# Kernel tuning notes

Hardware: AMD Instinct MI355X
Metric: run time of the kernel (lower is better)

## Reference

```python
import jax, jax.numpy as jnp
import numpy as np

B, N, D, H = 256, 1000, 128, 8
DH = D // H
TANH_CLIP = 10.0
NEG = -1e9  # finite stand-in for -inf mask fill (keeps grads clean)


def setup_inputs() -> dict:
    key = jax.random.key(0)
    ks = jax.random.split(key, 8)
    s = 1.0 / np.sqrt(D)
    return {
        "node_embeddings": jax.random.normal(ks[0], (B, N, D), jnp.float32),
        "W_node": jax.random.normal(ks[1], (D, 3 * D), jnp.float32) * s,   # project_node_embeddings
        "W_fixed": jax.random.normal(ks[2], (D, D), jnp.float32) * s,      # project_fixed_context
        "W_step": jax.random.normal(ks[3], (2 * D, D), jnp.float32) * s,   # project_step_context
        "W_out": jax.random.normal(ks[4], (D, D), jnp.float32) * s,        # project_out
        "prev_idx": jax.random.randint(ks[5], (B,), 0, N),
        "first_idx": jax.random.randint(ks[6], (B,), 0, N),
        "mask": jax.random.randint(ks[7], (B, N), 0, 2).astype(bool),      # True = masked/visited
    }


def reference(node_embeddings, W_node, W_fixed, W_step, W_out, prev_idx, first_idx, mask):
    b = jnp.arange(B)
    # Precompute fixed: context projection of graph embedding (mean aggregation)
    graph_embed = node_embeddings.mean(axis=1)                    # (B, D)
    fixed_context = graph_embed @ W_fixed                          # (B, D)
    # glimpse key / glimpse val / logit key from node embeddings
    kvl = node_embeddings @ W_node                                 # (B, N, 3D)
    glimpse_K, glimpse_V, logit_K = jnp.split(kvl, 3, axis=-1)
    gK = glimpse_K.reshape(B, N, H, DH)                            # (B, N, H, dh)
    gV = glimpse_V.reshape(B, N, H, DH)
    # Step context: cat(first node embed, last node embed) -> query
    step_ctx = jnp.concatenate(
        [node_embeddings[b, first_idx], node_embeddings[b, prev_idx]], axis=-1)  # (B, 2D)
    query = fixed_context + step_ctx @ W_step                      # (B, D)
    Q = query.reshape(B, H, DH)                                    # (B, H, dh)
    # Glimpse MHA (single query per batch element)
    compat = jnp.einsum("bhd,bnhd->bhn", Q, gK) / np.sqrt(DH)      # (B, H, N)
    compat = jnp.where(mask[:, None, :], NEG, compat)              # mask_inner
    attn = jax.nn.softmax(compat, axis=-1)
    heads = jnp.einsum("bhn,bnhd->bhd", attn, gV)                  # (B, H, dh)
    glimpse = heads.reshape(B, D) @ W_out                          # (B, D)
    # Logits against logit_K, tanh clipping, mask_logits, log-softmax
    logits = jnp.einsum("bd,bnd->bn", glimpse, logit_K) / np.sqrt(D)
    logits = TANH_CLIP * jnp.tanh(logits)
    logits = jnp.where(mask, NEG, logits)
    log_p = jax.nn.log_softmax(logits, axis=-1)                    # (B, N)
    return log_p
```

## Files before the change

### kernel.cpp

```cpp
#include <hip/hip_runtime.h>
#include <math.h>

#define BB 256
#define NN 1000
#define DD 128
#define HH 8
#define CC 8
#define RC 125
#define NEG -1e9f

__device__ __forceinline__ bool get_mask(const void* m, int flag, size_t idx) {
    if (flag == 1) return ((const int*)m)[idx] != 0;
    if (flag == 2) return ((const float*)m)[idx] != 0.0f;
    return ((const unsigned char*)m)[idx] != 0;
}

__global__ __launch_bounds__(256) void k_mean(
        const float* __restrict__ X, float* __restrict__ partial,
        const unsigned int* __restrict__ maskw, int* __restrict__ flag) {
    int bid = blockIdx.x, tid = threadIdx.x;
    int b = bid >> 3, ch = bid & 7;
    if (bid == 0 && tid < 64) {
        unsigned int a0 = maskw[tid], a1 = maskw[tid + 64],
                     a2 = maskw[tid + 128], a3 = maskw[tid + 192];
        int ii = (a0 <= 1u) && (a1 <= 1u) && (a2 <= 1u) && (a3 <= 1u);
        int ff = (a0 == 0u || a0 == 0x3F800000u) && (a1 == 0u || a1 == 0x3F800000u) &&
                 (a2 == 0u || a2 == 0x3F800000u) && (a3 == 0u || a3 == 0x3F800000u);
        int ai = __all(ii), af = __all(ff);
        if (tid == 0) *flag = ai ? 1 : (af ? 2 : 0);
    }
    int c = tid & 31, s = tid >> 5;
    const float4* Xr = (const float4*)(X + (size_t)b * NN * DD);
    float4 acc = make_float4(0.f, 0.f, 0.f, 0.f);
    int n0 = ch * RC;
    for (int nl = s; nl < RC; nl += 8) {
        float4 v = Xr[(n0 + nl) * 32 + c];
        acc.x += v.x; acc.y += v.y; acc.z += v.z; acc.w += v.w;
    }
    __shared__ float4 red[8][32];
    red[s][c] = acc;
    __syncthreads();
    for (int st = 4; st >= 1; st >>= 1) {
        if (s < st) {
            float4 o = red[s + st][c];
            red[s][c].x += o.x; red[s][c].y += o.y;
            red[s][c].z += o.z; red[s][c].w += o.w;
        }
        __syncthreads();
    }
    if (s == 0) {
        float4 r = red[0][c];
        float* outp = partial + ((size_t)b * CC + ch) * DD + 4 * c;
        outp[0] = r.x; outp[1] = r.y; outp[2] = r.z; outp[3] = r.w;
    }
}

__global__ __launch_bounds__(256) void k_qk(
        const float* __restrict__ X, const float* __restrict__ Wfix,
        const float* __restrict__ Wstep, const float* __restrict__ Wnode,
        const float* __restrict__ partial, const int* __restrict__ prev,
        const int* __restrict__ first, const void* __restrict__ mask,
        const int* __restrict__ flag, float* __restrict__ qkg,
        unsigned short* __restrict__ cidx, int* __restrict__ cnt) {
    int b = blockIdx.x, tid = threadIdx.x;
    const size_t xoff = (size_t)b * NN * DD;
    const int f = *flag;
    __shared__ float ge[DD], sc[2 * DD], qv[DD], qp[2][DD];
    __shared__ int wbase[4];
    __shared__ int s_total;

    if (tid < DD) {
        float g = 0.f;
        #pragma unroll
        for (int ch = 0; ch < CC; ++ch) g += partial[((size_t)b * CC + ch) * DD + tid];
        ge[tid] = g * (1.0f / NN);
    }
    {
        int src = (tid < DD) ? first[b] : prev[b];
        sc[tid] = X[xoff + (size_t)src * DD + (tid & 127)];
    }
    if (tid == 0) s_total = 0;
    __syncthreads();
    int p = tid >> 7, d = tid & 127;
    {
        float a = 0.f;
        #pragma unroll 4
        for (int k = p * 64; k < p * 64 + 64; ++k)      a += ge[k] * Wfix[(size_t)k * DD + d];
        #pragma unroll 4
        for (int k = p * 128; k < p * 128 + 128; ++k)   a += sc[k] * Wstep[(size_t)k * DD + d];
        qp[p][d] = a;
    }
    __syncthreads();
    if (tid < DD) qv[tid] = qp[0][tid] + qp[1][tid];
    __syncthreads();
    {
        const float* wrow = Wnode + (size_t)d * 384;
        #pragma unroll
        for (int h = p * 4; h < p * 4 + 4; ++h) {
            const float4* wr = (const float4*)(wrow + h * 16);
            float a = 0.f;
            #pragma unroll
            for (int j4 = 0; j4 < 4; ++j4) {
                float4 w = wr[j4];
                a += w.x * qv[h * 16 + 4 * j4]     + w.y * qv[h * 16 + 4 * j4 + 1]
                   + w.z * qv[h * 16 + 4 * j4 + 2] + w.w * qv[h * 16 + 4 * j4 + 3];
            }
            qkg[((size_t)b * HH + h) * DD + d] = 0.25f * a;
        }
    }
    int w = tid >> 6, lane = tid & 63;
    for (int seg = 0; seg < 4; ++seg) {
        int n = seg * 256 + tid;
        bool un = (n < NN) && !get_mask(mask, f, (size_t)b * NN + n);
        unsigned long long bal = __ballot(un);
        if (lane == 0) wbase[w] = __popcll(bal);
        __syncthreads();
        int base = s_total;
        for (int ww = 0; ww < w; ++ww) base += wbase[ww];
        int myoff = __popcll(bal & ((1ULL << lane) - 1ULL));
        if (un) cidx[(size_t)b * 1024 + base + myoff] = (unsigned short)n;
        __syncthreads();
        if (tid == 0) s_total += wbase[0] + wbase[1] + wbase[2] + wbase[3];
        __syncthreads();
    }
    if (tid == 0) cnt[b] = s_total;
}

__global__ __launch_bounds__(256, 4) void k_flash(
        const float* __restrict__ X, const float* __restrict__ qkg,
        const unsigned short* __restrict__ cidx, const int* __restrict__ cnt,
        float* __restrict__ sqw, float* __restrict__ pvp) {
    int bid = blockIdx.x, tid = threadIdx.x;
    int b = bid >> 3, ch = bid & 7;
    const size_t xoff = (size_t)b * NN * DD;

    __shared__ __align__(16) float qks[HH][DD];
    __shared__ __align__(16) float redpv[4][HH][DD];
    __shared__ float redS[4][HH];

    for (int i = tid; i < HH * DD; i += 256)
        qks[i >> 7][i & 127] = qkg[(size_t)b * HH * DD + i];
    __syncthreads();

    const int g = tid & 15;
    const int r = tid >> 4;
    const int w = tid >> 6;

    int total = cnt[b];
    int rpc = (total + CC - 1) / CC;
    int k0 = ch * rpc;
    int k1 = k0 + rpc; if (k1 > total) k1 = total;
    int len = k1 - k0; if (len < 0) len = 0;
    int iters = (len + 15) >> 4;

    float acc[HH][8];
    #pragma unroll
    for (int h = 0; h < HH; ++h)
        #pragma unroll
        for (int j = 0; j < 8; ++j) acc[h][j] = 0.f;
    float S[HH] = {0.f, 0.f, 0.f, 0.f, 0.f, 0.f, 0.f, 0.f};

    for (int it = 0; it < iters; ++it) {
        int k = k0 + it * 16 + r;
        if (k < k1) {
            int n = cidx[(size_t)b * 1024 + k];
            const float4* xr = (const float4*)(X + xoff + (size_t)n * DD + 8 * g);
            float4 v0 = xr[0], v1 = xr[1];
            float v[8] = {v0.x, v0.y, v0.z, v0.w, v1.x, v1.y, v1.z, v1.w};
            float cp[HH];
            #pragma unroll
            for (int h = 0; h < HH; ++h) {
                const float4* qr = (const float4*)&qks[h][8 * g];
                float4 q0 = qr[0], q1 = qr[1];
                cp[h] = v[0] * q0.x + v[1] * q0.y + v[2] * q0.z + v[3] * q0.w
                      + v[4] * q1.x + v[5] * q1.y + v[6] * q1.z + v[7] * q1.w;
            }
            #pragma unroll
            for (int h = 0; h < HH; ++h) {
                cp[h] += __shfl_xor(cp[h], 1, 16);
                cp[h] += __shfl_xor(cp[h], 2, 16);
                cp[h] += __shfl_xor(cp[h], 4, 16);
                cp[h] += __shfl_xor(cp[h], 8, 16);
            }
            #pragma unroll
            for (int h = 0; h < HH; ++h) {
                float pe = __expf(fminf(cp[h], 80.f));
                S[h] += pe;
                #pragma unroll
                for (int j = 0; j < 8; ++j) acc[h][j] += pe * v[j];
            }
        }
    }
    #pragma unroll
    for (int h = 0; h < HH; ++h) {
        S[h] += __shfl_xor(S[h], 16, 64);
        S[h] += __shfl_xor(S[h], 32, 64);
        #pragma unroll
        for (int j = 0; j < 8; ++j) {
            acc[h][j] += __shfl_xor(acc[h][j], 16, 64);
            acc[h][j] += __shfl_xor(acc[h][j], 32, 64);
        }
    }
    if ((tid & 63) < 16) {
        #pragma unroll
        for (int h = 0; h < HH; ++h) {
            *((float4*)&redpv[w][h][8 * g])     =
                make_float4(acc[h][0], acc[h][1], acc[h][2], acc[h][3]);
            *((float4*)&redpv[w][h][8 * g + 4]) =
                make_float4(acc[h][4], acc[h][5], acc[h][6], acc[h][7]);
        }
        if (g == 0) {
            #pragma unroll
            for (int h = 0; h < HH; ++h) redS[w][h] = S[h];
        }
    }
    __syncthreads();
    for (int idx = tid; idx < HH * DD; idx += 256) {
        int h = idx >> 7, d = idx & 127;
        pvp[(((size_t)b * CC + ch) * HH + h) * DD + d] =
            redpv[0][h][d] + redpv[1][h][d] + redpv[2][h][d] + redpv[3][h][d];
    }
    if (tid < HH)
        sqw[((size_t)b * CC + ch) * HH + tid] =
            redS[0][tid] + redS[1][tid] + redS[2][tid] + redS[3][tid];
}

__global__ __launch_bounds__(256) void k_comb(
        const float* __restrict__ Wnode, const float* __restrict__ Wout,
        const float* __restrict__ sqw, const float* __restrict__ pvp,
        float* __restrict__ gqg) {
    int b = blockIdx.x, tid = threadIdx.x;
    __shared__ float Sh[HH];
    __shared__ float xa[HH][DD], qp[2][DD], hd[DD], gl[DD];
    if (tid < HH) {
        float S = 0.f;
        #pragma unroll
        for (int ch = 0; ch < CC; ++ch) S += sqw[((size_t)b * CC + ch) * HH + tid];
        Sh[tid] = 1.0f / S;
    }
    __syncthreads();
    for (int idx = tid; idx < HH * DD; idx += 256) {
        int h = idx >> 7, d = idx & 127;
        float a = 0.f;
        #pragma unroll
        for (int ch = 0; ch < CC; ++ch)
            a += pvp[(((size_t)b * CC + ch) * HH + h) * DD + d];
        xa[h][d] = a * Sh[h];
    }
    __syncthreads();
    int p = tid >> 7, t = tid & 127;
    {
        int h = t >> 4;
        float a = 0.f;
        #pragma unroll 4
        for (int d = p * 64; d < p * 64 + 64; ++d)
            a += xa[h][d] * Wnode[(size_t)d * 384 + 128 + t];
        qp[p][t] = a;
    }
    __syncthreads();
    if (tid < DD) hd[tid] = qp[0][tid] + qp[1][tid];
    __syncthreads();
    {
        float a = 0.f;
        #pragma unroll 4
        for (int k = p * 64; k < p * 64 + 64; ++k) a += hd[k] * Wout[(size_t)k * DD + t];
        qp[p][t] = a;
    }
    __syncthreads();
    if (tid < DD) gl[tid] = qp[0][tid] + qp[1][tid];
    __syncthreads();
    {
        const float4* wr = (const float4*)(Wnode + (size_t)t * 384 + 256 + p * 64);
        float a = 0.f;
        #pragma unroll
        for (int j4 = 0; j4 < 16; ++j4) {
            float4 w = wr[j4];
            int k = p * 64 + 4 * j4;
            a += w.x * gl[k] + w.y * gl[k + 1] + w.z * gl[k + 2] + w.w * gl[k + 3];
        }
        qp[p][t] = a;
    }
    __syncthreads();
    if (tid < DD) gqg[(size_t)b * DD + tid] = (qp[0][tid] + qp[1][tid]) * 0.08838834764831845f;
}

__global__ __launch_bounds__(256, 8) void k_logits(
        const float* __restrict__ X, const float* __restrict__ gqg,
        const void* __restrict__ mask, const int* __restrict__ flag,
        const unsigned short* __restrict__ cidx, const int* __restrict__ cnt,
        float* __restrict__ lg, float* __restrict__ esumg) {
    int bid = blockIdx.x, tid = threadIdx.x;
    int b = bid >> 3, ch = bid & 7;
    const size_t xoff = (size_t)b * NN * DD;
    const int f = *flag;
    __shared__ float gqv[DD];
    __shared__ float redw[4];
    if (tid < DD) gqv[tid] = gqg[(size_t)b * DD + tid];
    __syncthreads();
    if (tid < RC) {
        int n = ch * RC + tid;
        if (get_mask(mask, f, (size_t)b * NN + n)) lg[(size_t)b * NN + n] = NEG;
    }
    int total = cnt[b];
    int rpc = (total + CC - 1) / CC;
    int k0 = ch * rpc, k1 = k0 + rpc; if (k1 > total) k1 = total;
    int len = k1 - k0; if (len < 0) len = 0;
    int iters = (len + 31) >> 5;
    int g = tid & 7, rr = tid >> 3;
    float esum = 0.f;
    for (int it = 0; it < iters; ++it) {
        int k = k0 + it * 32 + rr;
        if (k < k1) {
            int n = cidx[(size_t)b * 1024 + k];
            const float4* xr = (const float4*)(X + xoff + (size_t)n * DD);
            float a = 0.f;
            #pragma unroll
            for (int i = 0; i < 4; ++i) {
                float4 v = xr[g + 8 * i];
                int col = 4 * (g + 8 * i);
                a += v.x * gqv[col] + v.y * gqv[col + 1]
                   + v.z * gqv[col + 2] + v.w * gqv[col + 3];
            }
            a += __shfl_xor(a, 1, 8);
            a += __shfl_xor(a, 2, 8);
            a += __shfl_xor(a, 4, 8);
            if (g == 0) {
                float l = 10.0f * tanhf(a);
                lg[(size_t)b * NN + n] = l;
                esum += __expf(l - 10.0f);
            }
        }
    }
    #pragma unroll
    for (int off = 32; off >= 1; off >>= 1) esum += __shfl_xor(esum, off, 64);
    if ((tid & 63) == 0) redw[tid >> 6] = esum;
    __syncthreads();
    if (tid == 0) esumg[(size_t)b * CC + ch] = redw[0] + redw[1] + redw[2] + redw[3];
}

__global__ __launch_bounds__(256) void k_final(
        const float* __restrict__ lg, const float* __restrict__ esumg,
        float* __restrict__ out) {
    int b = blockIdx.x, tid = threadIdx.x;
    float s = 0.f;
    #pragma unroll
    for (int ch = 0; ch < CC; ++ch) s += esumg[(size_t)b * CC + ch];
    float lse = 10.0f + logf(s);
    for (int n = tid; n < NN; n += 256)
        out[(size_t)b * NN + n] = lg[(size_t)b * NN + n] - lse;
}

__global__ __launch_bounds__(1024) void k_mega(
        const float* __restrict__ X, const float* __restrict__ Wnode,
        const float* __restrict__ Wfix, const float* __restrict__ Wstep,
        const float* __restrict__ Wout, const int* __restrict__ prev,
        const int* __restrict__ first, const void* __restrict__ mask,
        float* __restrict__ out) {
    int b = blockIdx.x, tid = threadIdx.x;
    __shared__ __align__(16) float cm[HH * 1024];
    __shared__ __align__(16) float qkl[HH * DD];
    __shared__ __align__(16) float qpart[8 * DD];
    __shared__ float xa[HH * DD];
    __shared__ float ge[DD], q[DD], sc[2 * DD], hd[DD], gl[DD], gqv[DD];
    __shared__ float red[16], invh[8];
    __shared__ int s_flag;
    const size_t xoff = (size_t)b * NN * DD;

    if (tid < 64) {
        const unsigned int* mw = (const unsigned int*)mask;
        unsigned int a0 = mw[tid], a1 = mw[tid + 64], a2 = mw[tid + 128], a3 = mw[tid + 192];
        int ii = (a0 <= 1u) && (a1 <= 1u) && (a2 <= 1u) && (a3 <= 1u);
        int ff = (a0 == 0u || a0 == 0x3F800000u) && (a1 == 0u || a1 == 0x3F800000u) &&
                 (a2 == 0u || a2 == 0x3F800000u) && (a3 == 0u || a3 == 0x3F800000u);
        int ai = __all(ii), af = __all(ff);
        if (tid == 0) s_flag = ai ? 1 : (af ? 2 : 0);
    }
    if (tid >= 256 && tid < 512) {
        int t = tid - 256;
        int src = (t < DD) ? first[b] : prev[b];
        sc[t] = X[xoff + (size_t)src * DD + (t & 127)];
    }
    {
        float4* red4 = (float4*)cm;
        int c = tid & 31, s = tid >> 5;
        const float4* Xr = (const float4*)(X + xoff);
        float4 acc = make_float4(0.f, 0.f, 0.f, 0.f);
        for (int n = s; n < NN; n += 32) {
            float4 v = Xr[n * 32 + c];
            acc.x += v.x; acc.y += v.y; acc.z += v.z; acc.w += v.w;
        }
        red4[s * 32 + c] = acc;
        __syncthreads();
        for (int st = 16; st >= 1; st >>= 1) {
            if (s < st) {
                float4 o = red4[(s + st) * 32 + c];
                float4 r = red4[s * 32 + c];
                r.x += o.x; r.y += o.y; r.z += o.z; r.w += o.w;
                red4[s * 32 + c] = r;
            }
            __syncthreads();
        }
        if (s == 0) {
            float4 r = red4[c];
            ge[4 * c] = r.x * (1.0f / NN); ge[4 * c + 1] = r.y * (1.0f / NN);
            ge[4 * c + 2] = r.z * (1.0f / NN); ge[4 * c + 3] = r.w * (1.0f / NN);
        }
        __syncthreads();
    }
    const int flag = s_flag;
    {
        int p = tid >> 7, d = tid & 127;
        float a = 0.f;
        for (int k = p * 16; k < p * 16 + 16; ++k) a += ge[k] * Wfix[k * DD + d];
        for (int k = p * 32; k < p * 32 + 32; ++k) a += sc[k] * Wstep[k * DD + d];
        qpart[p * DD + d] = a;
        __syncthreads();
        if (tid < DD) {
            float s = 0.f;
            for (int pp = 0; pp < 8; ++pp) s += qpart[pp * DD + tid];
            q[tid] = s;
        }
        __syncthreads();
        int d2 = tid >> 3, h = tid & 7;
        const float4* wr = (const float4*)(Wnode + (size_t)d2 * 384 + h * 16);
        float a2 = 0.f;
        for (int j4 = 0; j4 < 4; ++j4) {
            float4 w = wr[j4];
            a2 += w.x * q[h * 16 + 4 * j4]     + w.y * q[h * 16 + 4 * j4 + 1]
                + w.z * q[h * 16 + 4 * j4 + 2] + w.w * q[h * 16 + 4 * j4 + 3];
        }
        qkl[h * DD + d2] = 0.25f * a2;
        __syncthreads();
    }
    {
        int g = tid & 7;
        for (int it = 0; it < 8; ++it) {
            int n = it * 128 + (tid >> 3);
            if (n < NN) {
                float acc[HH] = {0.f, 0.f, 0.f, 0.f, 0.f, 0.f, 0.f, 0.f};
                const float4* xr = (const float4*)(X + xoff + (size_t)n * DD);
                for (int i = 0; i < 4; ++i) {
                    float4 v = xr[g + 8 * i];
                    int col = 4 * (g + 8 * i);
                    for (int h = 0; h < HH; ++h)
                        acc[h] += v.x * qkl[h * DD + col]     + v.y * qkl[h * DD + col + 1]
                                + v.z * qkl[h * DD + col + 2] + v.w * qkl[h * DD + col + 3];
                }
                for (int h = 0; h < HH; ++h) {
                    acc[h] += __shfl_xor(acc[h], 1, 8);
                    acc[h] += __shfl_xor(acc[h], 2, 8);
                    acc[h] += __shfl_xor(acc[h], 4, 8);
                }
                float val = acc[0];
                for (int h = 1; h < HH; ++h) val = (g == h) ? acc[h] : val;
                bool mk = get_mask(mask, flag, (size_t)b * NN + n);
                cm[g * 1024 + n] = mk ? NEG : val;
            }
        }
        __syncthreads();
    }
    {
        int h = tid >> 7, lane = tid & 127;
        float mx = -INFINITY;
        for (int n = lane; n < NN; n += 128) mx = fmaxf(mx, cm[h * 1024 + n]);
        for (int off = 32; off >= 1; off >>= 1) mx = fmaxf(mx, __shfl_xor(mx, off, 64));
        if ((tid & 63) == 0) red[tid >> 6] = mx;
        __syncthreads();
        float m_h = fmaxf(red[2 * h], red[2 * h + 1]);
        float sm = 0.f;
        for (int n = lane; n < NN; n += 128) {
            float p = __expf(cm[h * 1024 + n] - m_h);
            cm[h * 1024 + n] = p;
            sm += p;
        }
        for (int off = 32; off >= 1; off >>= 1) sm += __shfl_xor(sm, off, 64);
        __syncthreads();
        if ((tid & 63) == 0) red[tid >> 6] = sm;
        __syncthreads();
        if (tid < HH) invh[tid] = 1.0f / (red[2 * tid] + red[2 * tid + 1]);
        __syncthreads();
    }
    {
        int s = tid >> 7, d = tid & 127;
        float acc[HH] = {0.f, 0.f, 0.f, 0.f, 0.f, 0.f, 0.f, 0.f};
        for (int n = s; n < NN; n += 8) {
            float x = X[xoff + (size_t)n * DD + d];
            for (int h = 0; h < HH; ++h) acc[h] += cm[h * 1024 + n] * x;
        }
        __syncthreads();
        float* xp = cm;
        for (int h = 0; h < HH; ++h) xp[(s * HH + h) * DD + d] = acc[h];
        __syncthreads();
        if (s == 0) {
            for (int h = 0; h < HH; ++h) {
                float t = 0.f;
                for (int ss = 0; ss < 8; ++ss) t += xp[(ss * HH + h) * DD + d];
                xa[h * DD + d] = t * invh[h];
            }
        }
        __syncthreads();
    }
    {
        int p = tid >> 7, t = tid & 127;
        int h = t >> 4;
        float a = 0.f;
        for (int d = p * 16; d < p * 16 + 16; ++d)
            a += xa[h * DD + d] * Wnode[(size_t)d * 384 + 128 + t];
        qpart[p * DD + t] = a;
        __syncthreads();
        if (tid < DD) {
            float s = 0.f;
            for (int pp = 0; pp < 8; ++pp) s += qpart[pp * DD + tid];
            hd[tid] = s;
        }
        __syncthreads();
        a = 0.f;
        for (int k = p * 16; k < p * 16 + 16; ++k) a += hd[k] * Wout[(size_t)k * DD + t];
        qpart[p * DD + t] = a;
        __syncthreads();
        if (tid < DD) {
            float s = 0.f;
            for (int pp = 0; pp < 8; ++pp) s += qpart[pp * DD + tid];
            gl[tid] = s;
        }
        __syncthreads();
        const float4* wr = (const float4*)(Wnode + (size_t)t * 384 + 256 + p * 16);
        a = 0.f;
        for (int j4 = 0; j4 < 4; ++j4) {
            float4 w = wr[j4];
            int k = p * 16 + 4 * j4;
            a += w.x * gl[k] + w.y * gl[k + 1] + w.z * gl[k + 2] + w.w * gl[k + 3];
        }
        qpart[p * DD + t] = a;
        __syncthreads();
        if (tid < DD) {
            float s = 0.f;
            for (int pp = 0; pp < 8; ++pp) s += qpart[pp * DD + tid];
            gqv[tid] = s * 0.08838834764831845f;
        }
        __syncthreads();
    }
    {
        float* lg = qkl;
        int g = tid & 7;
        for (int it = 0; it < 8; ++it) {
            int n = it * 128 + (tid >> 3);
            if (n < NN) {
                const float4* xr = (const float4*)(X + xoff + (size_t)n * DD);
                float a = 0.f;
                for (int i = 0; i < 4; ++i) {
                    float4 v = xr[g + 8 * i];
                    int col = 4 * (g + 8 * i);
                    a += v.x * gqv[col] + v.y * gqv[col + 1] + v.z * gqv[col + 2] + v.w * gqv[col + 3];
                }
                a += __shfl_xor(a, 1, 8);
                a += __shfl_xor(a, 2, 8);
                a += __shfl_xor(a, 4, 8);
                if (g == 0) {
                    float lgt = 10.0f * tanhf(a);
                    lg[n] = get_mask(mask, flag, (size_t)b * NN + n) ? NEG : lgt;
                }
            }
        }
        __syncthreads();
        float v = (tid < NN) ? lg[tid] : -INFINITY;
        float mx = v;
        for (int off = 32; off >= 1; off >>= 1) mx = fmaxf(mx, __shfl_xor(mx, off, 64));
        if ((tid & 63) == 0) red[tid >> 6] = mx;
        __syncthreads();
        float m = red[0];
        for (int w = 1; w < 16; ++w) m = fmaxf(m, red[w]);
        float e = (tid < NN) ? __expf(v - m) : 0.f;
        float sm = e;
        for (int off = 32; off >= 1; off >>= 1) sm += __shfl_xor(sm, off, 64);
        __syncthreads();
        if ((tid & 63) == 0) red[tid >> 6] = sm;
        __syncthreads();
        float s2 = 0.f;
        for (int w = 0; w < 16; ++w) s2 += red[w];
        float lse = m + logf(s2);
        if (tid < NN) out[(size_t)b * NN + tid] = v - lse;
    }
}

extern "C" void kernel_launch(void* const* d_in, const int* in_sizes, int n_in,
                              void* d_out, int out_size, void* d_ws, size_t ws_size,
                              hipStream_t stream) {
    const float* X     = (const float*)d_in[0];
    const float* Wnode = (const float*)d_in[1];
    const float* Wfix  = (const float*)d_in[2];
    const float* Wstep = (const float*)d_in[3];
    const float* Wout  = (const float*)d_in[4];
    const int*   prev  = (const int*)d_in[5];
    const int*   first = (const int*)d_in[6];
    const void*  mask  = d_in[7];
    float* out = (float*)d_out;

    char* wsb = (char*)d_ws;
    int*   flag    = (int*)wsb;
    float* partial = (float*)(wsb + 256);
    float* qkg     = partial + (size_t)BB * CC * DD;
    float* sqw     = qkg + (size_t)BB * HH * DD;
    float* pvp     = sqw + (size_t)BB * CC * HH;
    float* gqg     = pvp + (size_t)BB * CC * HH * DD;
    float* esumg   = gqg + (size_t)BB * DD;
    float* lg      = esumg + (size_t)BB * CC;
    int*   cnt     = (int*)(lg + (size_t)BB * NN);
    unsigned short* cidx = (unsigned short*)(cnt + BB);
    const size_t need = 256 + sizeof(float) * (
        (size_t)BB * CC * DD + (size_t)BB * HH * DD + (size_t)BB * CC * HH +
        (size_t)BB * CC * HH * DD + (size_t)BB * DD + (size_t)BB * CC + (size_t)BB * NN)
        + sizeof(int) * BB + sizeof(unsigned short) * (size_t)BB * 1024;

    if (ws_size >= need) {
        k_mean  <<<BB * CC, 256, 0, stream>>>(X, partial, (const unsigned int*)mask, flag);
        k_qk    <<<BB, 256, 0, stream>>>(X, Wfix, Wstep, Wnode, partial, prev, first,
                                         mask, flag, qkg, cidx, cnt);
        k_flash <<<BB * CC, 256, 0, stream>>>(X, qkg, cidx, cnt, sqw, pvp);
        k_comb  <<<BB, 256, 0, stream>>>(Wnode, Wout, sqw, pvp, gqg);
        k_logits<<<BB * CC, 256, 0, stream>>>(X, gqg, mask, flag, cidx, cnt, lg, esumg);
        k_final <<<BB, 256, 0, stream>>>(lg, esumg, out);
    } else {
        k_mega<<<BB, 1024, 0, stream>>>(X, Wnode, Wfix, Wstep, Wout,
                                        prev, first, mask, out);
    }
}
```

Before: 122.0 us.

## Fuse six-kernel pipeline into one persistent kernel with per-batch atomic flags

After: 107.5 us. 1.14x faster.

```diff
diff --git a/kernel.cpp b/kernel.cpp
--- a/kernel.cpp
+++ b/kernel.cpp
@@ -5,9 +5,15 @@
 #define NN 1000
 #define DD 128
 #define HH 8
-#define CC 8
-#define RC 125
+#define QQ 4
+#define RQ 250
 #define NEG -1e9f
+
+#define SY_CNTA 0
+#define SY_QK   1
+#define SY_CNTC 2
+#define SY_GQ   3
+#define SY_CNTE 4
 
 __device__ __forceinline__ bool get_mask(const void* m, int flag, size_t idx) {
     if (flag == 1) return ((const int*)m)[idx] != 0;
@@ -15,339 +21,343 @@
     return ((const unsigned char*)m)[idx] != 0;
 }
 
-__global__ __launch_bounds__(256) void k_mean(
-        const float* __restrict__ X, float* __restrict__ partial,
-        const unsigned int* __restrict__ maskw, int* __restrict__ flag) {
-    int bid = blockIdx.x, tid = threadIdx.x;
-    int b = bid >> 3, ch = bid & 7;
-    if (bid == 0 && tid < 64) {
-        unsigned int a0 = maskw[tid], a1 = maskw[tid + 64],
-                     a2 = maskw[tid + 128], a3 = maskw[tid + 192];
+__device__ __forceinline__ void sy_arrive(int* p) {
+    __builtin_amdgcn_fence(__ATOMIC_RELEASE, "agent");
+    __hip_atomic_fetch_add(p, 1, __ATOMIC_RELAXED, __HIP_MEMORY_SCOPE_AGENT);
+}
+__device__ __forceinline__ void sy_set(int* p) {
+    __builtin_amdgcn_fence(__ATOMIC_RELEASE, "agent");
+    __hip_atomic_store(p, 1, __ATOMIC_RELAXED, __HIP_MEMORY_SCOPE_AGENT);
+}
+__device__ __forceinline__ void sy_wait(int* p, int tgt) {
+    while (__hip_atomic_load(p, __ATOMIC_RELAXED, __HIP_MEMORY_SCOPE_AGENT) < tgt)
+        __builtin_amdgcn_s_sleep(8);
+    __builtin_amdgcn_fence(__ATOMIC_ACQUIRE, "agent");
+}
+
+__global__ __launch_bounds__(256, 4) void k_one(
+        const float* __restrict__ X, const float* __restrict__ Wnode,
+        const float* __restrict__ Wfix, const float* __restrict__ Wstep,
+        const float* __restrict__ Wout, const int* __restrict__ prev,
+        const int* __restrict__ first, const void* __restrict__ mask,
+        int* __restrict__ syg, float* __restrict__ partial,
+        float* __restrict__ qkg, float* __restrict__ sqw,
+        float* __restrict__ pvp, float* __restrict__ gqg,
+        float* __restrict__ esumg, float* __restrict__ out) {
+    const int bid = blockIdx.x, tid = threadIdx.x;
+    const int b = bid >> 2, q = bid & 3;
+    const int n0 = q * RQ;
+    const size_t xoff = (size_t)b * NN * DD;
+    int* sy = syg + b * 16;
+
+    __shared__ __align__(16) unsigned char pool[16384];
+    __shared__ __align__(16) float qks[HH][DD];
+    __shared__ float gqv[DD];
+    __shared__ float lgl[256];
+    __shared__ unsigned short cidxL[256];
+    __shared__ float redS[4][HH];
+    __shared__ float Sh[HH];
+    __shared__ float redw[4];
+    __shared__ int wbase[4];
+    __shared__ int s_flag, s_cnt;
+    float* poolf = (float*)pool;
+
+    if (tid < 64) {
+        const unsigned int* mw = (const unsigned int*)mask;
+        unsigned int a0 = mw[tid], a1 = mw[tid + 64], a2 = mw[tid + 128], a3 = mw[tid + 192];
         int ii = (a0 <= 1u) && (a1 <= 1u) && (a2 <= 1u) && (a3 <= 1u);
         int ff = (a0 == 0u || a0 == 0x3F800000u) && (a1 == 0u || a1 == 0x3F800000u) &&
                  (a2 == 0u || a2 == 0x3F800000u) && (a3 == 0u || a3 == 0x3F800000u);
         int ai = __all(ii), af = __all(ff);
-        if (tid == 0) *flag = ai ? 1 : (af ? 2 : 0);
-    }
-    int c = tid & 31, s = tid >> 5;
-    const float4* Xr = (const float4*)(X + (size_t)b * NN * DD);
-    float4 acc = make_float4(0.f, 0.f, 0.f, 0.f);
-    int n0 = ch * RC;
-    for (int nl = s; nl < RC; nl += 8) {
-        float4 v = Xr[(n0 + nl) * 32 + c];
-        acc.x += v.x; acc.y += v.y; acc.z += v.z; acc.w += v.w;
-    }
-    __shared__ float4 red[8][32];
-    red[s][c] = acc;
-    __syncthreads();
-    for (int st = 4; st >= 1; st >>= 1) {
-        if (s < st) {
-            float4 o = red[s + st][c];
-            red[s][c].x += o.x; red[s][c].y += o.y;
-            red[s][c].z += o.z; red[s][c].w += o.w;
-        }
-        __syncthreads();
-    }
-    if (s == 0) {
-        float4 r = red[0][c];
-        float* outp = partial + ((size_t)b * CC + ch) * DD + 4 * c;
-        outp[0] = r.x; outp[1] = r.y; outp[2] = r.z; outp[3] = r.w;
-    }
-}
-
-__global__ __launch_bounds__(256) void k_qk(
-        const float* __restrict__ X, const float* __restrict__ Wfix,
-        const float* __restrict__ Wstep, const float* __restrict__ Wnode,
-        const float* __restrict__ partial, const int* __restrict__ prev,
-        const int* __restrict__ first, const void* __restrict__ mask,
-        const int* __restrict__ flag, float* __restrict__ qkg,
-        unsigned short* __restrict__ cidx, int* __restrict__ cnt) {
-    int b = blockIdx.x, tid = threadIdx.x;
-    const size_t xoff = (size_t)b * NN * DD;
-    const int f = *flag;
-    __shared__ float ge[DD], sc[2 * DD], qv[DD], qp[2][DD];
-    __shared__ int wbase[4];
-    __shared__ int s_total;
-
-    if (tid < DD) {
-        float g = 0.f;
-        #pragma unroll
-        for (int ch = 0; ch < CC; ++ch) g += partial[((size_t)b * CC + ch) * DD + tid];
-        ge[tid] = g * (1.0f / NN);
-    }
-    {
-        int src = (tid < DD) ? first[b] : prev[b];
-        sc[tid] = X[xoff + (size_t)src * DD + (tid & 127)];
-    }
-    if (tid == 0) s_total = 0;
-    __syncthreads();
-    int p = tid >> 7, d = tid & 127;
-    {
-        float a = 0.f;
-        #pragma unroll 4
-        for (int k = p * 64; k < p * 64 + 64; ++k)      a += ge[k] * Wfix[(size_t)k * DD + d];
-        #pragma unroll 4
-        for (int k = p * 128; k < p * 128 + 128; ++k)   a += sc[k] * Wstep[(size_t)k * DD + d];
-        qp[p][d] = a;
-    }
-    __syncthreads();
-    if (tid < DD) qv[tid] = qp[0][tid] + qp[1][tid];
-    __syncthreads();
-    {
-        const float* wrow = Wnode + (size_t)d * 384;
-        #pragma unroll
-        for (int h = p * 4; h < p * 4 + 4; ++h) {
-            const float4* wr = (const float4*)(wrow + h * 16);
-            float a = 0.f;
-            #pragma unroll
-            for (int j4 = 0; j4 < 4; ++j4) {
-                float4 w = wr[j4];
-                a += w.x * qv[h * 16 + 4 * j4]     + w.y * qv[h * 16 + 4 * j4 + 1]
-                   + w.z * qv[h * 16 + 4 * j4 + 2] + w.w * qv[h * 16 + 4 * j4 + 3];
-            }
-            qkg[((size_t)b * HH + h) * DD + d] = 0.25f * a;
-        }
-    }
-    int w = tid >> 6, lane = tid & 63;
-    for (int seg = 0; seg < 4; ++seg) {
-        int n = seg * 256 + tid;
-        bool un = (n < NN) && !get_mask(mask, f, (size_t)b * NN + n);
+        if (tid == 0) s_flag = ai ? 1 : (af ? 2 : 0);
+    }
+
+    {
+        float4* red4 = (float4*)pool;
+        int c = tid & 31, s = tid >> 5;
+        const float4* Xr = (const float4*)(X + xoff);
+        float4 acc = make_float4(0.f, 0.f, 0.f, 0.f);
+        for (int nl = s; nl < RQ; nl += 8) {
+            float4 v = Xr[(n0 + nl) * 32 + c];
+            acc.x += v.x; acc.y += v.y; acc.z += v.z; acc.w += v.w;
+        }
+        red4[s * 32 + c] = acc;
+        __syncthreads();
+        for (int st = 4; st >= 1; st >>= 1) {
+            if (s < st) {
+                float4 o = red4[(s + st) * 32 + c];
+                float4 r = red4[s * 32 + c];
+                r.x += o.x; r.y += o.y; r.z += o.z; r.w += o.w;
+                red4[s * 32 + c] = r;
+            }
+            __syncthreads();
+        }
+        if (s == 0) {
+            float4 r = red4[c];
+            float* outp = partial + ((size_t)b * QQ + q) * DD + 4 * c;
+            outp[0] = r.x; outp[1] = r.y; outp[2] = r.z; outp[3] = r.w;
+        }
+    }
+    {
+        int w = tid >> 6, lane = tid & 63;
+        bool un = (tid < RQ) && !get_mask(mask, s_flag, (size_t)b * NN + n0 + tid);
         unsigned long long bal = __ballot(un);
         if (lane == 0) wbase[w] = __popcll(bal);
         __syncthreads();
-        int base = s_total;
+        int base = 0;
         for (int ww = 0; ww < w; ++ww) base += wbase[ww];
-        int myoff = __popcll(bal & ((1ULL << lane) - 1ULL));
-        if (un) cidx[(size_t)b * 1024 + base + myoff] = (unsigned short)n;
-        __syncthreads();
-        if (tid == 0) s_total += wbase[0] + wbase[1] + wbase[2] + wbase[3];
-        __syncthreads();
-    }
-    if (tid == 0) cnt[b] = s_total;
-}
-
-__global__ __launch_bounds__(256, 4) void k_flash(
-        const float* __restrict__ X, const float* __restrict__ qkg,
-        const unsigned short* __restrict__ cidx, const int* __restrict__ cnt,
-        float* __restrict__ sqw, float* __restrict__ pvp) {
-    int bid = blockIdx.x, tid = threadIdx.x;
-    int b = bid >> 3, ch = bid & 7;
-    const size_t xoff = (size_t)b * NN * DD;
-
-    __shared__ __align__(16) float qks[HH][DD];
-    __shared__ __align__(16) float redpv[4][HH][DD];
-    __shared__ float redS[4][HH];
-
+        int off = __popcll(bal & ((1ULL << lane) - 1ULL));
+        if (un) cidxL[base + off] = (unsigned short)tid;
+        if (tid == 0) s_cnt = wbase[0] + wbase[1] + wbase[2] + wbase[3];
+    }
+    __syncthreads();
+    if (tid == 0) sy_arrive(&sy[SY_CNTA]);
+
+    if (q == 0) {
+        if (tid == 0) sy_wait(&sy[SY_CNTA], QQ);
+        __syncthreads();
+        float* ge = poolf;
+        float* sc = poolf + 128;
+        float* qv = poolf + 384;
+        float* qp = poolf + 512;
+        if (tid < DD) {
+            float g = 0.f;
+            #pragma unroll
+            for (int qq = 0; qq < QQ; ++qq) g += partial[((size_t)b * QQ + qq) * DD + tid];
+            ge[tid] = g * (1.0f / NN);
+        }
+        {
+            int src = (tid < DD) ? first[b] : prev[b];
+            sc[tid] = X[xoff + (size_t)src * DD + (tid & 127)];
+        }
+        __syncthreads();
+        int p = tid >> 7, d = tid & 127;
+        {
+            float a = 0.f;
+            #pragma unroll 4
+            for (int k = p * 64; k < p * 64 + 64; ++k)      a += ge[k] * Wfix[(size_t)k * DD + d];
+            #pragma unroll 4
+            for (int k = p * 128; k < p * 128 + 128; ++k)   a += sc[k] * Wstep[(size_t)k * DD + d];
+            qp[p * DD + d] = a;
+        }
+        __syncthreads();
+        if (tid < DD) qv[tid] = qp[tid] + qp[DD + tid];
+        __syncthreads();
+        {
+            const float* wrow = Wnode + (size_t)d * 384;
+            #pragma unroll
+            for (int h = p * 4; h < p * 4 + 4; ++h) {
+                const float4* wr = (const float4*)(wrow + h * 16);
+                float a = 0.f;
+                #pragma unroll
+                for (int j4 = 0; j4 < 4; ++j4) {
+                    float4 w = wr[j4];
+                    a += w.x * qv[h * 16 + 4 * j4]     + w.y * qv[h * 16 + 4 * j4 + 1]
+                       + w.z * qv[h * 16 + 4 * j4 + 2] + w.w * qv[h * 16 + 4 * j4 + 3];
+                }
+                qkg[((size_t)b * HH + h) * DD + d] = 0.25f * a;
+            }
+        }
+        __syncthreads();
+        if (tid == 0) sy_set(&sy[SY_QK]);
+    }
+    if (tid == 0) sy_wait(&sy[SY_QK], 1);
+    __syncthreads();
     for (int i = tid; i < HH * DD; i += 256)
         qks[i >> 7][i & 127] = qkg[(size_t)b * HH * DD + i];
     __syncthreads();
 
-    const int g = tid & 15;
-    const int r = tid >> 4;
-    const int w = tid >> 6;
-
-    int total = cnt[b];
-    int rpc = (total + CC - 1) / CC;
-    int k0 = ch * rpc;
-    int k1 = k0 + rpc; if (k1 > total) k1 = total;
-    int len = k1 - k0; if (len < 0) len = 0;
-    int iters = (len + 15) >> 4;
-
-    float acc[HH][8];
-    #pragma unroll
-    for (int h = 0; h < HH; ++h)
+    {
+        float* redpv = poolf;
+        const int g = tid & 15, r = tid >> 4, w = tid >> 6;
+        int len = s_cnt;
+        int iters = (len + 15) >> 4;
+        float acc[HH][8];
         #pragma unroll
-        for (int j = 0; j < 8; ++j) acc[h][j] = 0.f;
-    float S[HH] = {0.f, 0.f, 0.f, 0.f, 0.f, 0.f, 0.f, 0.f};
-
-    for (int it = 0; it < iters; ++it) {
-        int k = k0 + it * 16 + r;
-        if (k < k1) {
-            int n = cidx[(size_t)b * 1024 + k];
-            const float4* xr = (const float4*)(X + xoff + (size_t)n * DD + 8 * g);
-            float4 v0 = xr[0], v1 = xr[1];
-            float v[8] = {v0.x, v0.y, v0.z, v0.w, v1.x, v1.y, v1.z, v1.w};
-            float cp[HH];
-            #pragma unroll
-            for (int h = 0; h < HH; ++h) {
-                const float4* qr = (const float4*)&qks[h][8 * g];
-                float4 q0 = qr[0], q1 = qr[1];
-                cp[h] = v[0] * q0.x + v[1] * q0.y + v[2] * q0.z + v[3] * q0.w
-                      + v[4] * q1.x + v[5] * q1.y + v[6] * q1.z + v[7] * q1.w;
-            }
-            #pragma unroll
-            for (int h = 0; h < HH; ++h) {
-                cp[h] += __shfl_xor(cp[h], 1, 16);
-                cp[h] += __shfl_xor(cp[h], 2, 16);
-                cp[h] += __shfl_xor(cp[h], 4, 16);
-                cp[h] += __shfl_xor(cp[h], 8, 16);
-            }
-            #pragma unroll
-            for (int h = 0; h < HH; ++h) {
-                float pe = __expf(fminf(cp[h], 80.f));
-                S[h] += pe;
+        for (int h = 0; h < HH; ++h)
+            #pragma unroll
+            for (int j = 0; j < 8; ++j) acc[h][j] = 0.f;
+        float S[HH] = {0.f, 0.f, 0.f, 0.f, 0.f, 0.f, 0.f, 0.f};
+
+        for (int it = 0; it < iters; ++it) {
+            int k = it * 16 + r;
+            if (k < len) {
+                int n = n0 + cidxL[k];
+                const float4* xr = (const float4*)(X + xoff + (size_t)n * DD + 8 * g);
+                float4 v0 = xr[0], v1 = xr[1];
+                float v[8] = {v0.x, v0.y, v0.z, v0.w, v1.x, v1.y, v1.z, v1.w};
+                float cp[HH];
                 #pragma unroll
-                for (int j = 0; j < 8; ++j) acc[h][j] += pe * v[j];
-            }
-        }
-    }
-    #pragma unroll
-    for (int h = 0; h < HH; ++h) {
-        S[h] += __shfl_xor(S[h], 16, 64);
-        S[h] += __shfl_xor(S[h], 32, 64);
-        #pragma unroll
-        for (int j = 0; j < 8; ++j) {
-            acc[h][j] += __shfl_xor(acc[h][j], 16, 64);
-            acc[h][j] += __shfl_xor(acc[h][j], 32, 64);
-        }
-    }
-    if ((tid & 63) < 16) {
+                for (int h = 0; h < HH; ++h) {
+                    const float4* qr = (const float4*)&qks[h][8 * g];
+                    float4 q0 = qr[0], q1 = qr[1];
+                    cp[h] = v[0] * q0.x + v[1] * q0.y + v[2] * q0.z + v[3] * q0.w
+                          + v[4] * q1.x + v[5] * q1.y + v[6] * q1.z + v[7] * q1.w;
+                }
+                #pragma unroll
+                for (int h = 0; h < HH; ++h) {
+                    cp[h] += __shfl_xor(cp[h], 1, 16);
+                    cp[h] += __shfl_xor(cp[h], 2, 16);
+                    cp[h] += __shfl_xor(cp[h], 4, 16);
+                    cp[h] += __shfl_xor(cp[h], 8, 16);
+                }
+                #pragma unroll
+                for (int h = 0; h < HH; ++h) {
+                    float pe = __expf(fminf(cp[h], 80.f));
+                    S[h] += pe;
+                    #pragma unroll
+                    for (int j = 0; j < 8; ++j) acc[h][j] += pe * v[j];
+                }
+            }
+        }
         #pragma unroll
         for (int h = 0; h < HH; ++h) {
-            *((float4*)&redpv[w][h][8 * g])     =
-                make_float4(acc[h][0], acc[h][1], acc[h][2], acc[h][3]);
-            *((float4*)&redpv[w][h][8 * g + 4]) =
-                make_float4(acc[h][4], acc[h][5], acc[h][6], acc[h][7]);
-        }
-        if (g == 0) {
-            #pragma unroll
-            for (int h = 0; h < HH; ++h) redS[w][h] = S[h];
-        }
-    }
-    __syncthreads();
-    for (int idx = tid; idx < HH * DD; idx += 256) {
-        int h = idx >> 7, d = idx & 127;
-        pvp[(((size_t)b * CC + ch) * HH + h) * DD + d] =
-            redpv[0][h][d] + redpv[1][h][d] + redpv[2][h][d] + redpv[3][h][d];
-    }
-    if (tid < HH)
-        sqw[((size_t)b * CC + ch) * HH + tid] =
-            redS[0][tid] + redS[1][tid] + redS[2][tid] + redS[3][tid];
-}
-
-__global__ __launch_bounds__(256) void k_comb(
-        const float* __restrict__ Wnode, const float* __restrict__ Wout,
-        const float* __restrict__ sqw, const float* __restrict__ pvp,
-        float* __restrict__ gqg) {
-    int b = blockIdx.x, tid = threadIdx.x;
-    __shared__ float Sh[HH];
-    __shared__ float xa[HH][DD], qp[2][DD], hd[DD], gl[DD];
-    if (tid < HH) {
-        float S = 0.f;
+            S[h] += __shfl_xor(S[h], 16, 64);
+            S[h] += __shfl_xor(S[h], 32, 64);
+            #pragma unroll
+            for (int j = 0; j < 8; ++j) {
+                acc[h][j] += __shfl_xor(acc[h][j], 16, 64);
+                acc[h][j] += __shfl_xor(acc[h][j], 32, 64);
+            }
+        }
+        if ((tid & 63) < 16) {
+            #pragma unroll
+            for (int h = 0; h < HH; ++h) {
+                *((float4*)&redpv[((size_t)w * HH + h) * DD + 8 * g]) =
+                    make_float4(acc[h][0], acc[h][1], acc[h][2], acc[h][3]);
+                *((float4*)&redpv[((size_t)w * HH + h) * DD + 8 * g + 4]) =
+                    make_float4(acc[h][4], acc[h][5], acc[h][6], acc[h][7]);
+            }
+            if (g == 0) {
+                #pragma unroll
+                for (int h = 0; h < HH; ++h) redS[w][h] = S[h];
+            }
+        }
+        __syncthreads();
+        for (int idx = tid; idx < HH * DD; idx += 256) {
+            int h = idx >> 7, d = idx & 127;
+            pvp[(((size_t)b * QQ + q) * HH + h) * DD + d] =
+                redpv[(0 * HH + h) * DD + d] + redpv[(1 * HH + h) * DD + d] +
+                redpv[(2 * HH + h) * DD + d] + redpv[(3 * HH + h) * DD + d];
+        }
+        if (tid < HH)
+            sqw[((size_t)b * QQ + q) * HH + tid] =
+                redS[0][tid] + redS[1][tid] + redS[2][tid] + redS[3][tid];
+    }
+    __syncthreads();
+    if (tid == 0) sy_arrive(&sy[SY_CNTC]);
+
+    if (q == 0) {
+        if (tid == 0) sy_wait(&sy[SY_CNTC], QQ);
+        __syncthreads();
+        float* xa = poolf;
+        float* hd = poolf + 1024;
+        float* gl = poolf + 1152;
+        float* qp = poolf + 1280;
+        if (tid < HH) {
+            float S = 0.f;
+            #pragma unroll
+            for (int qq = 0; qq < QQ; ++qq) S += sqw[((size_t)b * QQ + qq) * HH + tid];
+            Sh[tid] = 1.0f / S;
+        }
+        __syncthreads();
+        for (int idx = tid; idx < HH * DD; idx += 256) {
+            int h = idx >> 7, d = idx & 127;
+            float a = 0.f;
+            #pragma unroll
+            for (int qq = 0; qq < QQ; ++qq)
+                a += pvp[(((size_t)b * QQ + qq) * HH + h) * DD + d];
+            xa[h * DD + d] = a * Sh[h];
+        }
+        __syncthreads();
+        int p = tid >> 7, t = tid & 127;
+        {
+            int h = t >> 4;
+            float a = 0.f;
+            #pragma unroll 4
+            for (int d = p * 64; d < p * 64 + 64; ++d)
+                a += xa[h * DD + d] * Wnode[(size_t)d * 384 + 128 + t];
+            qp[p * DD + t] = a;
+        }
+        __syncthreads();
+        if (tid < DD) hd[tid] = qp[tid] + qp[DD + tid];
+        __syncthreads();
+        {
+            float a = 0.f;
+            #pragma unroll 4
+            for (int k = p * 64; k < p * 64 + 64; ++k) a += hd[k] * Wout[(size_t)k * DD + t];
+            qp[p * DD + t] = a;
+        }
+        __syncthreads();
+        if (tid < DD) gl[tid] = qp[tid] + qp[DD + tid];
+        __syncthreads();
+        {
+            const float4* wr = (const float4*)(Wnode + (size_t)t * 384 + 256 + p * 64);
+            float a = 0.f;
+            #pragma unroll
+            for (int j4 = 0; j4 < 16; ++j4) {
+                float4 w = wr[j4];
+                int k = p * 64 + 4 * j4;
+                a += w.x * gl[k] + w.y * gl[k + 1] + w.z * gl[k + 2] + w.w * gl[k + 3];
+            }
+            qp[p * DD + t] = a;
+        }
+        __syncthreads();
+        if (tid < DD)
+            gqg[(size_t)b * DD + tid] = (qp[tid] + qp[DD + tid]) * 0.08838834764831845f;
+        __syncthreads();
+        if (tid == 0) sy_set(&sy[SY_GQ]);
+    }
+    if (tid == 0) sy_wait(&sy[SY_GQ], 1);
+    __syncthreads();
+    if (tid < DD) gqv[tid] = gqg[(size_t)b * DD + tid];
+    if (tid < RQ) lgl[tid] = NEG;
+    __syncthreads();
+
+    {
+        int len = s_cnt;
+        int g = tid & 7, rr = tid >> 3;
+        int iters = (len + 31) >> 5;
+        float esum = 0.f;
+        for (int it = 0; it < iters; ++it) {
+            int k = it * 32 + rr;
+            if (k < len) {
+                int nl = cidxL[k];
+                const float4* xr = (const float4*)(X + xoff + (size_t)(n0 + nl) * DD);
+                float a = 0.f;
+                #pragma unroll
+                for (int i = 0; i < 4; ++i) {
+                    float4 v = xr[g + 8 * i];
+                    int col = 4 * (g + 8 * i);
+                    a += v.x * gqv[col] + v.y * gqv[col + 1]
+                       + v.z * gqv[col + 2] + v.w * gqv[col + 3];
+                }
+                a += __shfl_xor(a, 1, 8);
+                a += __shfl_xor(a, 2, 8);
+                a += __shfl_xor(a, 4, 8);
+                if (g == 0) {
+                    float l = 10.0f * tanhf(a);
+                    lgl[nl] = l;
+                    esum += __expf(l - 10.0f);
+                }
+            }
+        }
         #pragma unroll
-        for (int ch = 0; ch < CC; ++ch) S += sqw[((size_t)b * CC + ch) * HH + tid];
-        Sh[tid] = 1.0f / S;
-    }
-    __syncthreads();
-    for (int idx = tid; idx < HH * DD; idx += 256) {
-        int h = idx >> 7, d = idx & 127;
-        float a = 0.f;
-        #pragma unroll
-        for (int ch = 0; ch < CC; ++ch)
-            a += pvp[(((size_t)b * CC + ch) * HH + h) * DD + d];
-        xa[h][d] = a * Sh[h];
-    }
-    __syncthreads();
-    int p = tid >> 7, t = tid & 127;
-    {
-        int h = t >> 4;
-        float a = 0.f;
-        #pragma unroll 4
-        for (int d = p * 64; d < p * 64 + 64; ++d)
-            a += xa[h][d] * Wnode[(size_t)d * 384 + 128 + t];
-        qp[p][t] = a;
-    }
-    __syncthreads();
-    if (tid < DD) hd[tid] = qp[0][tid] + qp[1][tid];
-    __syncthreads();
-    {
-        float a = 0.f;
-        #pragma unroll 4
-        for (int k = p * 64; k < p * 64 + 64; ++k) a += hd[k] * Wout[(size_t)k * DD + t];
-        qp[p][t] = a;
-    }
-    __syncthreads();
-    if (tid < DD) gl[tid] = qp[0][tid] + qp[1][tid];
-    __syncthreads();
-    {
-        const float4* wr = (const float4*)(Wnode + (size_t)t * 384 + 256 + p * 64);
-        float a = 0.f;
-        #pragma unroll
-        for (int j4 = 0; j4 < 16; ++j4) {
-            float4 w = wr[j4];
-            int k = p * 64 + 4 * j4;
-            a += w.x * gl[k] + w.y * gl[k + 1] + w.z * gl[k + 2] + w.w * gl[k + 3];
-        }
-        qp[p][t] = a;
-    }
-    __syncthreads();
-    if (tid < DD) gqg[(size_t)b * DD + tid] = (qp[0][tid] + qp[1][tid]) * 0.08838834764831845f;
-}
-
-__global__ __launch_bounds__(256, 8) void k_logits(
-        const float* __restrict__ X, const float* __restrict__ gqg,
-        const void* __restrict__ mask, const int* __restrict__ flag,
-        const unsigned short* __restrict__ cidx, const int* __restrict__ cnt,
-        float* __restrict__ lg, float* __restrict__ esumg) {
-    int bid = blockIdx.x, tid = threadIdx.x;
-    int b = bid >> 3, ch = bid & 7;
-    const size_t xoff = (size_t)b * NN * DD;
-    const int f = *flag;
-    __shared__ float gqv[DD];
-    __shared__ float redw[4];
-    if (tid < DD) gqv[tid] = gqg[(size_t)b * DD + tid];
-    __syncthreads();
-    if (tid < RC) {
-        int n = ch * RC + tid;
-        if (get_mask(mask, f, (size_t)b * NN + n)) lg[(size_t)b * NN + n] = NEG;
-    }
-    int total = cnt[b];
-    int rpc = (total + CC - 1) / CC;
-    int k0 = ch * rpc, k1 = k0 + rpc; if (k1 > total) k1 = total;
-    int len = k1 - k0; if (len < 0) len = 0;
-    int iters = (len + 31) >> 5;
-    int g = tid & 7, rr = tid >> 3;
-    float esum = 0.f;
-    for (int it = 0; it < iters; ++it) {
-        int k = k0 + it * 32 + rr;
-        if (k < k1) {
-            int n = cidx[(size_t)b * 1024 + k];
-            const float4* xr = (const float4*)(X + xoff + (size_t)n * DD);
-            float a = 0.f;
-            #pragma unroll
-            for (int i = 0; i < 4; ++i) {
-                float4 v = xr[g + 8 * i];
-                int col = 4 * (g + 8 * i);
-                a += v.x * gqv[col] + v.y * gqv[col + 1]
-                   + v.z * gqv[col + 2] + v.w * gqv[col + 3];
-            }
-            a += __shfl_xor(a, 1, 8);
-            a += __shfl_xor(a, 2, 8);
-            a += __shfl_xor(a, 4, 8);
-            if (g == 0) {
-                float l = 10.0f * tanhf(a);
-                lg[(size_t)b * NN + n] = l;
-                esum += __expf(l - 10.0f);
-            }
-        }
-    }
-    #pragma unroll
-    for (int off = 32; off >= 1; off >>= 1) esum += __shfl_xor(esum, off, 64);
-    if ((tid & 63) == 0) redw[tid >> 6] = esum;
-    __syncthreads();
-    if (tid == 0) esumg[(size_t)b * CC + ch] = redw[0] + redw[1] + redw[2] + redw[3];
-}
-
-__global__ __launch_bounds__(256) void k_final(
-        const float* __restrict__ lg, const float* __restrict__ esumg,
-        float* __restrict__ out) {
-    int b = blockIdx.x, tid = threadIdx.x;
-    float s = 0.f;
-    #pragma unroll
-    for (int ch = 0; ch < CC; ++ch) s += esumg[(size_t)b * CC + ch];
-    float lse = 10.0f + logf(s);
-    for (int n = tid; n < NN; n += 256)
-        out[(size_t)b * NN + n] = lg[(size_t)b * NN + n] - lse;
+        for (int off = 32; off >= 1; off >>= 1) esum += __shfl_xor(esum, off, 64);
+        if ((tid & 63) == 0) redw[tid >> 6] = esum;
+        __syncthreads();
+        if (tid == 0) esumg[(size_t)b * QQ + q] = redw[0] + redw[1] + redw[2] + redw[3];
+    }
+    __syncthreads();
+    if (tid == 0) { sy_arrive(&sy[SY_CNTE]); sy_wait(&sy[SY_CNTE], QQ); }
+    __syncthreads();
+
+    {
+        float s = esumg[(size_t)b * QQ] + esumg[(size_t)b * QQ + 1]
+                + esumg[(size_t)b * QQ + 2] + esumg[(size_t)b * QQ + 3];
+        float lse = 10.0f + logf(s);
+        if (tid < RQ) out[(size_t)b * NN + n0 + tid] = lgl[tid] - lse;
+    }
 }
 
 __global__ __launch_bounds__(1024) void k_mega(
@@ -597,29 +607,27 @@
     float* out = (float*)d_out;
 
     char* wsb = (char*)d_ws;
-    int*   flag    = (int*)wsb;
-    float* partial = (float*)(wsb + 256);
-    float* qkg     = partial + (size_t)BB * CC * DD;
+    int*   syg     = (int*)wsb;
+    float* partial = (float*)(wsb + 16384);
+    float* qkg     = partial + (size_t)BB * QQ * DD;
     float* sqw     = qkg + (size_t)BB * HH * DD;
-    float* pvp     = sqw + (size_t)BB * CC * HH;
-    float* gqg     = pvp + (size_t)BB * CC * HH * DD;
+    float* pvp     = sqw + (size_t)BB * QQ * HH;
+    float* gqg     = pvp + (size_t)BB * QQ * HH * DD;
     float* esumg   = gqg + (size_t)BB * DD;
-    float* lg      = esumg + (size_t)BB * CC;
-    int*   cnt     = (int*)(lg + (size_t)BB * NN);
-    unsigned short* cidx = (unsigned short*)(cnt + BB);
-    const size_t need = 256 + sizeof(float) * (
-        (size_t)BB * CC * DD + (size_t)BB * HH * DD + (size_t)BB * CC * HH +
-        (size_t)BB * CC * HH * DD + (size_t)BB * DD + (size_t)BB * CC + (size_t)BB * NN)
-        + sizeof(int) * BB + sizeof(unsigned short) * (size_t)BB * 1024;
-
-    if (ws_size >= need) {
-        k_mean  <<<BB * CC, 256, 0, stream>>>(X, partial, (const unsigned int*)mask, flag);
-        k_qk    <<<BB, 256, 0, stream>>>(X, Wfix, Wstep, Wnode, partial, prev, first,
-                                         mask, flag, qkg, cidx, cnt);
-        k_flash <<<BB * CC, 256, 0, stream>>>(X, qkg, cidx, cnt, sqw, pvp);
-        k_comb  <<<BB, 256, 0, stream>>>(Wnode, Wout, sqw, pvp, gqg);
-        k_logits<<<BB * CC, 256, 0, stream>>>(X, gqg, mask, flag, cidx, cnt, lg, esumg);
-        k_final <<<BB, 256, 0, stream>>>(lg, esumg, out);
+    const size_t need = 16384 + sizeof(float) * (
+        (size_t)BB * QQ * DD + (size_t)BB * HH * DD + (size_t)BB * QQ * HH +
+        (size_t)BB * QQ * HH * DD + (size_t)BB * DD + (size_t)BB * QQ);
+
+    int maxb = 0;
+    bool ok = (ws_size >= need) &&
+              (hipOccupancyMaxActiveBlocksPerMultiprocessor(&maxb, (const void*)k_one,
+                                                            256, 0) == hipSuccess) &&
+              (maxb >= QQ);
+    if (ok) {
+        hipMemsetAsync(syg, 0, 16384, stream);
+        k_one<<<BB * QQ, 256, 0, stream>>>(X, Wnode, Wfix, Wstep, Wout, prev, first,
+                                           mask, syg, partial, qkg, sqw, pvp, gqg,
+                                           esumg, out);
     } else {
         k_mega<<<BB, 1024, 0, stream>>>(X, Wnode, Wfix, Wstep, Wout,
                                         prev, first, mask, out);
```
